# Optimization experiments

Measured on AMD Instinct MI355X. Metric: run time of the kernel, lower is better.

The kernel has to match this reference:

```python
import jax, jax.numpy as jnp
import numpy as np

N_NODES = 100000
N_EDGES = 3200000
D_FEAT = 128
UNITS = 128
EPS = 0.0


def setup_inputs() -> dict:
    key = jax.random.key(0)
    k1, k2, k3, k4, k5 = jax.random.split(key, 5)
    X = jax.random.normal(k1, (N_NODES, D_FEAT), dtype=jnp.float32)
    ref_A = jax.random.randint(k2, (N_EDGES,), 0, N_NODES, dtype=jnp.int32)  # dst per edge
    ref_B = jax.random.randint(k3, (N_EDGES,), 0, N_NODES, dtype=jnp.int32)  # src per edge
    # Glorot-uniform weights, zero biases (as in build())
    lim1 = float(np.sqrt(6.0 / (D_FEAT + UNITS)))
    lim2 = float(np.sqrt(6.0 / (UNITS + UNITS)))
    w1 = jax.random.uniform(k4, (D_FEAT, UNITS), minval=-lim1, maxval=lim1, dtype=jnp.float32)
    b1 = jnp.zeros((UNITS,), dtype=jnp.float32)
    w2 = jax.random.uniform(k5, (UNITS, UNITS), minval=-lim2, maxval=lim2, dtype=jnp.float32)
    b2 = jnp.zeros((UNITS,), dtype=jnp.float32)
    return {"X": X, "ref_A": ref_A, "ref_B": ref_B, "w1": w1, "b1": b1, "w2": w2, "b2": b2}


def reference(X, ref_A, ref_B, w1, b1, w2, b2):
    # c.convolution: gather source-node features and scatter-add to destinations
    agg = jax.ops.segment_sum(X[ref_B], ref_A, num_segments=N_NODES)  # [N, d]
    conv_X = (1.0 + EPS) * X + agg
    h = jax.nn.relu(conv_X @ w1 + b1)  # [N, units]
    out = jax.nn.relu(h @ w2 + b2)     # [N, units]
    return out
```

## Files before the change

kernel.cpp:

```cpp
#include <hip/hip_runtime.h>
#include <hip/hip_bf16.h>

#define NNODES 100000
#define DFEAT 128
#define NBKT 8
#define STRIPE 12500
#define BUCKET_CAP 416000
#define CHUNK 4096
#define SUBNODES 64
#define NSUB 196
#define SUBCAP 2560
#define NSB (NBKT * NSUB)
#define NBIN (SUBNODES * 16)

typedef short bf16x8 __attribute__((ext_vector_type(8)));
typedef float f32x4  __attribute__((ext_vector_type(4)));

__device__ __forceinline__ unsigned short f2bf(float f) {
    unsigned u = __builtin_bit_cast(unsigned, f);
    return (unsigned short)((u + 0x7fffu + ((u >> 16) & 1u)) >> 16);
}

__global__ __launch_bounds__(256)
void prep_all(const float4* __restrict__ X, uint4* __restrict__ Xb, int n8, int n8b,
              const float* __restrict__ w1, const float* __restrict__ w2,
              unsigned short* __restrict__ w1t, unsigned short* __restrict__ w2t,
              int* __restrict__ zbase) {
    const int bid = blockIdx.x;
    const int tid = threadIdx.x;
    if (bid < n8b) {
        int i = bid * 256 + tid;
        if (i >= n8) return;
        float4 a = X[2 * i], b = X[2 * i + 1];
        uint4 o;
        o.x = f2bf(a.x) | ((unsigned)f2bf(a.y) << 16);
        o.y = f2bf(a.z) | ((unsigned)f2bf(a.w) << 16);
        o.z = f2bf(b.x) | ((unsigned)f2bf(b.y) << 16);
        o.w = f2bf(b.z) | ((unsigned)f2bf(b.w) << 16);
        Xb[i] = o;
    } else if (bid < n8b + 128) {
        int i = (bid - n8b) * 256 + tid;
        const float* w = (i < 16384) ? w1 : w2;
        unsigned short* o = (i < 16384) ? w1t : w2t;
        int j = i & 16383;
        int n = j >> 7, k = j & 127;
        o[n * 128 + k] = f2bf(w[k * 128 + n]);
    } else {
        for (int i = tid; i < 64 + NSB; i += 256) zbase[i] = 0;
    }
}

__global__ __launch_bounds__(256)
void partition_edges(const int* __restrict__ dst, const int* __restrict__ src,
                     int* __restrict__ bcur, unsigned* __restrict__ bedges,
                     int nE) {
    __shared__ unsigned sbuf[CHUNK];
    __shared__ int scnt[NBKT];
    __shared__ int sbase[NBKT];
    __shared__ int scur[NBKT];
    __shared__ int gbase[NBKT];

    const int tid = threadIdx.x;
    const long long e0 = (long long)blockIdx.x * CHUNK;
    const int n = (int)min((long long)CHUNK, (long long)nE - e0);
    if (n <= 0) return;

    if (tid < NBKT) scnt[tid] = 0;
    __syncthreads();

    unsigned ent[CHUNK / 256];
    int bkt[CHUNK / 256];
#pragma unroll
    for (int j = 0; j < CHUNK / 256; ++j) {
        int i = tid + j * 256;
        if (i < n) {
            int d = dst[e0 + i];
            int s = src[e0 + i];
            int b = d / STRIPE;
            ent[j] = (unsigned)s | ((unsigned)(d - b * STRIPE) << 17);
            bkt[j] = b;
            atomicAdd(&scnt[b], 1);
        } else bkt[j] = -1;
    }
    __syncthreads();

    if (tid == 0) {
        int run = 0;
        for (int b = 0; b < NBKT; ++b) { sbase[b] = run; scur[b] = run; run += scnt[b]; }
    }
    __syncthreads();

#pragma unroll
    for (int j = 0; j < CHUNK / 256; ++j)
        if (bkt[j] >= 0) {
            int p = atomicAdd(&scur[bkt[j]], 1);
            sbuf[p] = ent[j];
        }
    if (tid < NBKT) gbase[tid] = atomicAdd(&bcur[tid], scnt[tid]);
    __syncthreads();

    for (int i = tid; i < n; i += 256) {
        int b = 0;
        while (b < NBKT - 1 && i >= sbase[b + 1]) ++b;
        bedges[(size_t)b * BUCKET_CAP + gbase[b] + (i - sbase[b])] = sbuf[i];
    }
}

__global__ __launch_bounds__(256)
void partition_sub(const unsigned* __restrict__ bedges, const int* __restrict__ bcur,
                   int* __restrict__ scur2, unsigned* __restrict__ sub_edges) {
    __shared__ unsigned sbuf[CHUNK];
    __shared__ int scnt[NSUB];
    __shared__ int sbase[NSUB + 1];
    __shared__ int scur[NSUB];
    __shared__ int gbase[NSUB];

    const int b   = blockIdx.x & (NBKT - 1);
    const int blk = blockIdx.x >> 3;
    const int sz  = bcur[b];
    const int e0  = blk * CHUNK;
    if (e0 >= sz) return;
    const int n = min(CHUNK, sz - e0);
    const unsigned* p = bedges + (size_t)b * BUCKET_CAP + e0;
    const int tid = threadIdx.x;

    for (int i = tid; i < NSUB; i += 256) scnt[i] = 0;
    __syncthreads();

    unsigned ent[CHUNK / 256];
    int sbk[CHUNK / 256];
#pragma unroll
    for (int j = 0; j < CHUNK / 256; ++j) {
        int i = tid + j * 256;
        if (i < n) {
            unsigned v = p[i];
            int s = (int)(v >> 23);
            ent[j] = v;
            sbk[j] = s;
            atomicAdd(&scnt[s], 1);
        } else sbk[j] = -1;
    }
    __syncthreads();

    if (tid == 0) {
        int run = 0;
        for (int s = 0; s < NSUB; ++s) { sbase[s] = run; scur[s] = run; run += scnt[s]; }
        sbase[NSUB] = run;
    }
    __syncthreads();

#pragma unroll
    for (int j = 0; j < CHUNK / 256; ++j)
        if (sbk[j] >= 0) {
            int pos = atomicAdd(&scur[sbk[j]], 1);
            sbuf[pos] = ent[j];
        }
    if (tid < NSUB) gbase[tid] = atomicAdd(&scur2[b * NSUB + tid], scnt[tid]);
    __syncthreads();

    const int wave = tid >> 6, lane = tid & 63;
    for (int s = wave; s < NSUB; s += 4) {
        int lo = sbase[s], hi = sbase[s + 1];
        if (lo == hi) continue;
        int g0 = gbase[s];
        unsigned* q = sub_edges + (size_t)(b * NSUB + s) * SUBCAP;
        for (int i = lo + lane; i < hi; i += 64) {
            int o = g0 + (i - lo);
            if (o < SUBCAP) q[o] = sbuf[i];
        }
    }
}

__device__ __forceinline__ void bfadd(float* acc, uint4 v) {
    acc[0] += __builtin_bit_cast(float, v.x << 16);
    acc[1] += __builtin_bit_cast(float, v.x & 0xffff0000u);
    acc[2] += __builtin_bit_cast(float, v.y << 16);
    acc[3] += __builtin_bit_cast(float, v.y & 0xffff0000u);
    acc[4] += __builtin_bit_cast(float, v.z << 16);
    acc[5] += __builtin_bit_cast(float, v.z & 0xffff0000u);
    acc[6] += __builtin_bit_cast(float, v.w << 16);
    acc[7] += __builtin_bit_cast(float, v.w & 0xffff0000u);
}

__global__ __launch_bounds__(256, 8)
void sort_aggregate(const unsigned* __restrict__ sub_edges,
                    const int* __restrict__ scur2,
                    const uint4* __restrict__ Xb, uint4* __restrict__ convb) {
    __shared__ unsigned srt[SUBCAP];
    __shared__ int cnt[NBIN];
    __shared__ int off[NBIN + 1];
    __shared__ int tmp[256];

    const int b  = blockIdx.x & (NBKT - 1);
    const int j  = blockIdx.x >> 3;
    const int sb = b * NSUB + j;
    const int tid = threadIdx.x;
    const int sz = min(scur2[sb], SUBCAP);
    const int nodeBase = b * STRIPE + j * SUBNODES;
    const int nLoc = min(SUBNODES, STRIPE - j * SUBNODES);
    const unsigned* p = sub_edges + (size_t)sb * SUBCAP;

#pragma unroll
    for (int q = 0; q < 4; ++q) cnt[tid * 4 + q] = 0;
    __syncthreads();
    for (int i = tid; i < sz; i += 256) {
        unsigned v = p[i];
        int key = (int)(((v >> 17) & 63) << 4) | (int)((v & 0x1FFFFu) >> 13);
        atomicAdd(&cnt[key], 1);
    }
    __syncthreads();

    int c0 = cnt[tid * 4], c1 = cnt[tid * 4 + 1],
        c2 = cnt[tid * 4 + 2], c3 = cnt[tid * 4 + 3];
    int tot = c0 + c1 + c2 + c3;
    tmp[tid] = tot;
    __syncthreads();
    for (int d = 1; d < 256; d <<= 1) {
        int t = (tid >= d) ? tmp[tid - d] : 0;
        __syncthreads();
        tmp[tid] += t;
        __syncthreads();
    }
    int base = tmp[tid] - tot;
    off[tid * 4 + 0] = base;
    off[tid * 4 + 1] = base + c0;
    off[tid * 4 + 2] = base + c0 + c1;
    off[tid * 4 + 3] = base + c0 + c1 + c2;
    if (tid == 255) off[NBIN] = tmp[255];
    __syncthreads();
#pragma unroll
    for (int q = 0; q < 4; ++q) cnt[tid * 4 + q] = off[tid * 4 + q];
    __syncthreads();

    for (int i = tid; i < sz; i += 256) {
        unsigned v = p[i];
        unsigned s = v & 0x1FFFFu;
        int key = (int)(((v >> 17) & 63) << 4) | (int)(s >> 13);
        int pos = atomicAdd(&cnt[key], 1);
        srt[pos] = s;
    }
    __syncthreads();

    const int grp = tid >> 4, lane = tid & 15;
    for (int n0 = grp; n0 < nLoc; n0 += 16) {
        int node = nodeBase + n0;
        float acc[8];
#pragma unroll
        for (int q = 0; q < 8; ++q) acc[q] = 0.f;
        bfadd(acc, Xb[(size_t)node * 16 + lane]);

        int e = off[n0 << 4], end = off[(n0 + 1) << 4];
        for (; e + 4 <= end; e += 4) {
            int s0 = srt[e + 0], s1 = srt[e + 1], s2 = srt[e + 2], s3 = srt[e + 3];
            uint4 v0 = Xb[(size_t)s0 * 16 + lane];
            uint4 v1 = Xb[(size_t)s1 * 16 + lane];
            uint4 v2 = Xb[(size_t)s2 * 16 + lane];
            uint4 v3 = Xb[(size_t)s3 * 16 + lane];
            bfadd(acc, v0); bfadd(acc, v1); bfadd(acc, v2); bfadd(acc, v3);
        }
        for (; e < end; ++e)
            bfadd(acc, Xb[(size_t)srt[e] * 16 + lane]);

        uint4 o;
        o.x = f2bf(acc[0]) | ((unsigned)f2bf(acc[1]) << 16);
        o.y = f2bf(acc[2]) | ((unsigned)f2bf(acc[3]) << 16);
        o.z = f2bf(acc[4]) | ((unsigned)f2bf(acc[5]) << 16);
        o.w = f2bf(acc[6]) | ((unsigned)f2bf(acc[7]) << 16);
        convb[(size_t)node * 16 + lane] = o;
    }
}

#define TM 128

__global__ __launch_bounds__(256, 2)
void mlp_fused(const unsigned short* __restrict__ convb,
               const unsigned short* __restrict__ w1t, const float* __restrict__ b1,
               const unsigned short* __restrict__ w2t, const float* __restrict__ b2,
               float* __restrict__ out, int N) {
    __shared__ unsigned short sA[TM][136];
    __shared__ unsigned short sW[128][136];

    const int tid  = threadIdx.x;
    const int row0 = blockIdx.x * TM;

    for (int i = tid; i < TM * 16; i += 256) {
        int r = i >> 4, c = i & 15;
        uint4 v = make_uint4(0, 0, 0, 0);
        if (row0 + r < N) v = ((const uint4*)convb)[(size_t)(row0 + r) * 16 + c];
        *(uint4*)&sA[r][c * 8] = v;
    }
    for (int i = tid; i < 128 * 16; i += 256) {
        int r = i >> 4, c = i & 15;
        *(uint4*)&sW[r][c * 8] = ((const uint4*)w1t)[r * 16 + c];
    }
    __syncthreads();

    const int lane = tid & 63;
    const int lrow = lane & 15;
    const int kgrp = lane >> 4;
    const int m0   = (tid >> 6) * 32;

    float bias[8];
#pragma unroll
    for (int nf = 0; nf < 8; ++nf) bias[nf] = b1[nf * 16 + lrow];

    f32x4 acc[2][8] = {};
#pragma unroll
    for (int kk = 0; kk < 128; kk += 32) {
        bf16x8 a0 = *(const bf16x8*)&sA[m0 + lrow][kk + kgrp * 8];
        bf16x8 a1 = *(const bf16x8*)&sA[m0 + 16 + lrow][kk + kgrp * 8];
#pragma unroll
        for (int nf = 0; nf < 8; ++nf) {
            bf16x8 b = *(const bf16x8*)&sW[nf * 16 + lrow][kk + kgrp * 8];
            acc[0][nf] = __builtin_amdgcn_mfma_f32_16x16x32_bf16(a0, b, acc[0][nf], 0, 0, 0);
            acc[1][nf] = __builtin_amdgcn_mfma_f32_16x16x32_bf16(a1, b, acc[1][nf], 0, 0, 0);
        }
    }

#pragma unroll
    for (int mf = 0; mf < 2; ++mf)
#pragma unroll
        for (int nf = 0; nf < 8; ++nf)
#pragma unroll
            for (int r = 0; r < 4; ++r) {
                int row = m0 + mf * 16 + kgrp * 4 + r;
                int col = nf * 16 + lrow;
                float h = fmaxf(acc[mf][nf][r] + bias[nf], 0.f);
                sA[row][col] = f2bf(h);
            }

    __syncthreads();

    for (int i = tid; i < 128 * 16; i += 256) {
        int r = i >> 4, c = i & 15;
        *(uint4*)&sW[r][c * 8] = ((const uint4*)w2t)[r * 16 + c];
    }
#pragma unroll
    for (int nf = 0; nf < 8; ++nf) bias[nf] = b2[nf * 16 + lrow];
#pragma unroll
    for (int mf = 0; mf < 2; ++mf)
#pragma unroll
        for (int nf = 0; nf < 8; ++nf) acc[mf][nf] = (f32x4){0.f, 0.f, 0.f, 0.f};
    __syncthreads();

#pragma unroll
    for (int kk = 0; kk < 128; kk += 32) {
        bf16x8 a0 = *(const bf16x8*)&sA[m0 + lrow][kk + kgrp * 8];
        bf16x8 a1 = *(const bf16x8*)&sA[m0 + 16 + lrow][kk + kgrp * 8];
#pragma unroll
        for (int nf = 0; nf < 8; ++nf) {
            bf16x8 b = *(const bf16x8*)&sW[nf * 16 + lrow][kk + kgrp * 8];
            acc[0][nf] = __builtin_amdgcn_mfma_f32_16x16x32_bf16(a0, b, acc[0][nf], 0, 0, 0);
            acc[1][nf] = __builtin_amdgcn_mfma_f32_16x16x32_bf16(a1, b, acc[1][nf], 0, 0, 0);
        }
    }

#pragma unroll
    for (int mf = 0; mf < 2; ++mf)
#pragma unroll
        for (int nf = 0; nf < 8; ++nf)
#pragma unroll
            for (int r = 0; r < 4; ++r) {
                int row = row0 + m0 + mf * 16 + kgrp * 4 + r;
                int col = nf * 16 + lrow;
                if (row < N)
                    out[(size_t)row * 128 + col] = fmaxf(acc[mf][nf][r] + bias[nf], 0.f);
            }
}

extern "C" void kernel_launch(void* const* d_in, const int* in_sizes, int n_in,
                              void* d_out, int out_size, void* d_ws, size_t ws_size,
                              hipStream_t stream) {
    const float* X    = (const float*)d_in[0];
    const int*   refA = (const int*)d_in[1];
    const int*   refB = (const int*)d_in[2];
    const float* w1   = (const float*)d_in[3];
    const float* b1   = (const float*)d_in[4];
    const float* w2   = (const float*)d_in[5];
    const float* b2   = (const float*)d_in[6];
    float* out = (float*)d_out;

    const int nNodes = in_sizes[0] / DFEAT;
    const int nE     = in_sizes[1];

    char* ws = (char*)d_ws;
    unsigned short* Xb    = (unsigned short*)ws;  ws += (size_t)nNodes * DFEAT * 2;
    unsigned short* convb = (unsigned short*)ws;
    unsigned* bedges      = (unsigned*)convb;
    ws += (size_t)nNodes * DFEAT * 2;
    unsigned* sub_edges = (unsigned*)ws;          ws += (size_t)NSB * SUBCAP * 4;
    unsigned short* w1t = (unsigned short*)ws;    ws += 16384 * 2;
    unsigned short* w2t = (unsigned short*)ws;    ws += 16384 * 2;
    int* bcur  = (int*)ws;                        ws += 64 * 4;
    int* scur2 = (int*)ws;

    int n8  = nNodes * DFEAT / 8;
    int n8b = (n8 + 255) / 256;
    prep_all<<<n8b + 128 + 1, 256, 0, stream>>>((const float4*)X, (uint4*)Xb, n8, n8b,
                                                w1, w2, w1t, w2t, bcur);

    int pBlocks = (nE + CHUNK - 1) / CHUNK;
    partition_edges<<<pBlocks, 256, 0, stream>>>(refA, refB, bcur, bedges, nE);
    partition_sub<<<(BUCKET_CAP / CHUNK + 1) * NBKT, 256, 0, stream>>>(
        bedges, bcur, scur2, sub_edges);

    sort_aggregate<<<NSB, 256, 0, stream>>>(sub_edges, scur2,
                                            (const uint4*)Xb, (uint4*)convb);

    int mBlocks = (nNodes + TM - 1) / TM;
    mlp_fused<<<mBlocks, 256, 0, stream>>>(convb, w1t, b1, w2t, b2, out, nNodes);
}
```

Measured before the change: 210.5 us.

## Sort edges slab-major and gather four nodes per group in lockstep by source slab

The counting-sort key becomes source-slab-major (13 slabs of 8192 source rows) instead of node-major. Each 16-lane group now owns four destination nodes and walks the slabs in order, interleaving gathers for all four nodes. Within a slab, all groups in the block fetch source rows from the same 8192-row region at roughly the same time, which is meant to improve cache locality and raise memory-level parallelism. In exchange it keeps four accumulator sets per thread, so occupancy is lowered to 4 blocks per SM, and groups whose four nodes have uneven edge counts run predicated idle iterations.

```diff
diff --git a/kernel.cpp b/kernel.cpp
--- a/kernel.cpp
+++ b/kernel.cpp
@@ -11,7 +11,9 @@
 #define NSUB 196
 #define SUBCAP 2560
 #define NSB (NBKT * NSUB)
-#define NBIN (SUBNODES * 16)
+#define NSLAB 13
+#define NBIN (NSLAB * SUBNODES)
+#define NBINP 1024
 
 typedef short bf16x8 __attribute__((ext_vector_type(8)));
 typedef float f32x4  __attribute__((ext_vector_type(4)));
@@ -182,12 +184,22 @@
     acc[7] += __builtin_bit_cast(float, v.w & 0xffff0000u);
 }
 
-__global__ __launch_bounds__(256, 8)
+__device__ __forceinline__ void packout(uint4* convb, int node, int lane,
+                                        const float* acc) {
+    uint4 o;
+    o.x = f2bf(acc[0]) | ((unsigned)f2bf(acc[1]) << 16);
+    o.y = f2bf(acc[2]) | ((unsigned)f2bf(acc[3]) << 16);
+    o.z = f2bf(acc[4]) | ((unsigned)f2bf(acc[5]) << 16);
+    o.w = f2bf(acc[6]) | ((unsigned)f2bf(acc[7]) << 16);
+    convb[(size_t)node * 16 + lane] = o;
+}
+
+__global__ __launch_bounds__(256, 4)
 void sort_aggregate(const unsigned* __restrict__ sub_edges,
                     const int* __restrict__ scur2,
                     const uint4* __restrict__ Xb, uint4* __restrict__ convb) {
     __shared__ unsigned srt[SUBCAP];
-    __shared__ int cnt[NBIN];
+    __shared__ int cnt[NBINP];
     __shared__ int off[NBIN + 1];
     __shared__ int tmp[256];
 
@@ -205,7 +217,7 @@
     __syncthreads();
     for (int i = tid; i < sz; i += 256) {
         unsigned v = p[i];
-        int key = (int)(((v >> 17) & 63) << 4) | (int)((v & 0x1FFFFu) >> 13);
+        int key = (int)((v & 0x1FFFFu) >> 13) * SUBNODES + (int)((v >> 17) & 63);
         atomicAdd(&cnt[key], 1);
     }
     __syncthreads();
@@ -222,52 +234,54 @@
         __syncthreads();
     }
     int base = tmp[tid] - tot;
-    off[tid * 4 + 0] = base;
-    off[tid * 4 + 1] = base + c0;
-    off[tid * 4 + 2] = base + c0 + c1;
-    off[tid * 4 + 3] = base + c0 + c1 + c2;
-    if (tid == 255) off[NBIN] = tmp[255];
-    __syncthreads();
-#pragma unroll
-    for (int q = 0; q < 4; ++q) cnt[tid * 4 + q] = off[tid * 4 + q];
+    int k = tid * 4;
+    int b0 = base, b1 = base + c0, b2 = base + c0 + c1, b3 = base + c0 + c1 + c2;
+    if (k     <= NBIN) off[k]     = b0;
+    if (k + 1 <= NBIN) off[k + 1] = b1;
+    if (k + 2 <= NBIN) off[k + 2] = b2;
+    if (k + 3 <= NBIN) off[k + 3] = b3;
+    __syncthreads();
+    cnt[k] = b0; cnt[k + 1] = b1; cnt[k + 2] = b2; cnt[k + 3] = b3;
     __syncthreads();
 
     for (int i = tid; i < sz; i += 256) {
         unsigned v = p[i];
         unsigned s = v & 0x1FFFFu;
-        int key = (int)(((v >> 17) & 63) << 4) | (int)(s >> 13);
+        int key = (int)(s >> 13) * SUBNODES + (int)((v >> 17) & 63);
         int pos = atomicAdd(&cnt[key], 1);
         srt[pos] = s;
     }
     __syncthreads();
 
     const int grp = tid >> 4, lane = tid & 15;
-    for (int n0 = grp; n0 < nLoc; n0 += 16) {
-        int node = nodeBase + n0;
-        float acc[8];
-#pragma unroll
-        for (int q = 0; q < 8; ++q) acc[q] = 0.f;
-        bfadd(acc, Xb[(size_t)node * 16 + lane]);
-
-        int e = off[n0 << 4], end = off[(n0 + 1) << 4];
-        for (; e + 4 <= end; e += 4) {
-            int s0 = srt[e + 0], s1 = srt[e + 1], s2 = srt[e + 2], s3 = srt[e + 3];
-            uint4 v0 = Xb[(size_t)s0 * 16 + lane];
-            uint4 v1 = Xb[(size_t)s1 * 16 + lane];
-            uint4 v2 = Xb[(size_t)s2 * 16 + lane];
-            uint4 v3 = Xb[(size_t)s3 * 16 + lane];
-            bfadd(acc, v0); bfadd(acc, v1); bfadd(acc, v2); bfadd(acc, v3);
-        }
-        for (; e < end; ++e)
-            bfadd(acc, Xb[(size_t)srt[e] * 16 + lane]);
-
-        uint4 o;
-        o.x = f2bf(acc[0]) | ((unsigned)f2bf(acc[1]) << 16);
-        o.y = f2bf(acc[2]) | ((unsigned)f2bf(acc[3]) << 16);
-        o.z = f2bf(acc[4]) | ((unsigned)f2bf(acc[5]) << 16);
-        o.w = f2bf(acc[6]) | ((unsigned)f2bf(acc[7]) << 16);
-        convb[(size_t)node * 16 + lane] = o;
-    }
+    const int n0 = grp, n1 = grp + 16, n2 = grp + 32, n3 = grp + 48;
+    float a0[8], a1[8], a2[8], a3[8];
+#pragma unroll
+    for (int q = 0; q < 8; ++q) { a0[q] = 0.f; a1[q] = 0.f; a2[q] = 0.f; a3[q] = 0.f; }
+    if (n0 < nLoc) bfadd(a0, Xb[(size_t)(nodeBase + n0) * 16 + lane]);
+    if (n1 < nLoc) bfadd(a1, Xb[(size_t)(nodeBase + n1) * 16 + lane]);
+    if (n2 < nLoc) bfadd(a2, Xb[(size_t)(nodeBase + n2) * 16 + lane]);
+    if (n3 < nLoc) bfadd(a3, Xb[(size_t)(nodeBase + n3) * 16 + lane]);
+
+    for (int s = 0; s < NSLAB; ++s) {
+        const int kb = s * SUBNODES;
+        int e0 = off[kb + n0], x0 = off[kb + n0 + 1];
+        int e1 = off[kb + n1], x1 = off[kb + n1 + 1];
+        int e2 = off[kb + n2], x2 = off[kb + n2 + 1];
+        int e3 = off[kb + n3], x3 = off[kb + n3 + 1];
+        int m = max(max(x0 - e0, x1 - e1), max(x2 - e2, x3 - e3));
+        for (int t = 0; t < m; ++t) {
+            if (e0 + t < x0) bfadd(a0, Xb[(size_t)srt[e0 + t] * 16 + lane]);
+            if (e1 + t < x1) bfadd(a1, Xb[(size_t)srt[e1 + t] * 16 + lane]);
+            if (e2 + t < x2) bfadd(a2, Xb[(size_t)srt[e2 + t] * 16 + lane]);
+            if (e3 + t < x3) bfadd(a3, Xb[(size_t)srt[e3 + t] * 16 + lane]);
+        }
+    }
+
+    if (n0 < nLoc) packout(convb, nodeBase + n0, lane, a0);
+    if (n1 < nLoc) packout(convb, nodeBase + n1, lane, a1);
+    if (n2 < nLoc) packout(convb, nodeBase + n2, lane, a2);
+    if (n3 < nLoc) packout(convb, nodeBase + n3, lane, a3);
 }
 
 #define TM 128
```

After: 202.8 us. 1.04x faster.
